# Performance work log

Measured on AMD Instinct MI355X. Metric: run time of the kernel, lower is better.

The kernel has to match this reference:

```python
import jax, jax.numpy as jnp
import numpy as np

N = 10000      # nodes
E = 160000     # directed edges (self loops added inside reference)
IN = 512       # input_len
HID = 256      # hidden per-head dim (hard-coded in module)
OUT = 128      # dim
H = 4          # heads
NEG_SLOPE = 0.2


def setup_inputs() -> dict:
    key = jax.random.key(0)
    ks = jax.random.split(key, 10)
    s = 0.05
    return {
        "x": jax.random.normal(ks[0], (N, IN), dtype=jnp.float32),
        "edge_index": jax.random.randint(ks[1], (2, E), 0, N, dtype=jnp.int64),
        # layer 1 params: GATv2Conv(IN, HID, heads=H, concat=False)
        "Wl1": jax.random.normal(ks[2], (IN, H * HID), dtype=jnp.float32) * s,
        "Wr1": jax.random.normal(ks[3], (IN, H * HID), dtype=jnp.float32) * s,
        "att1": jax.random.normal(ks[4], (H, HID), dtype=jnp.float32) * s,
        "b1": jnp.zeros((HID,), dtype=jnp.float32),
        # layer 2 params: GATv2Conv(HID, OUT, heads=H, concat=False)
        "Wl2": jax.random.normal(ks[5], (HID, H * OUT), dtype=jnp.float32) * s,
        "Wr2": jax.random.normal(ks[6], (HID, H * OUT), dtype=jnp.float32) * s,
        "att2": jax.random.normal(ks[7], (H, OUT), dtype=jnp.float32) * s,
        "b2": jnp.zeros((OUT,), dtype=jnp.float32),
    }


def gatv2_layer(x, src, dst, Wl, Wr, att, bias, num_nodes):
    """PyG GATv2Conv with concat=False (mean over heads), negative_slope=0.2."""
    heads, c = att.shape
    xl = (x @ Wl).reshape(num_nodes, heads, c)   # source transform
    xr = (x @ Wr).reshape(num_nodes, heads, c)   # target transform
    # per-edge attention logits: a^T LeakyReLU(xl[src] + xr[dst])  -> [E, H]
    e = jax.nn.leaky_relu(xl[src] + xr[dst], negative_slope=NEG_SLOPE)
    logits = jnp.einsum('ehc,hc->eh', e, att)
    # segment softmax over incoming edges of each destination node
    m = jax.ops.segment_max(logits, dst, num_segments=num_nodes)   # [N, H]
    ea = jnp.exp(logits - m[dst])
    denom = jax.ops.segment_sum(ea, dst, num_segments=num_nodes)   # [N, H]
    alpha = ea / denom[dst]                                        # [E, H]
    # scatter-aggregate messages
    out = jax.ops.segment_sum(alpha[:, :, None] * xl[src], dst, num_segments=num_nodes)
    return out.mean(axis=1) + bias                                 # [N, C]


def reference(x, edge_index, Wl1, Wr1, att1, b1, Wl2, Wr2, att2, b2):
    num_nodes = x.shape[0]
    loop = jnp.arange(num_nodes, dtype=edge_index.dtype)
    src = jnp.concatenate([edge_index[0], loop])
    dst = jnp.concatenate([edge_index[1], loop])
    h1 = jax.nn.leaky_relu(gatv2_layer(x, src, dst, Wl1, Wr1, att1, b1, num_nodes),
                           negative_slope=NEG_SLOPE)
    h2 = jnp.tanh(gatv2_layer(h1, src, dst, Wl2, Wr2, att2, b2, num_nodes))
    return h2
```

## Files before the change

kernel.cpp:

```cpp
#include <hip/hip_runtime.h>
#include <hip/hip_bf16.h>
#include <math.h>

#define DEVINL __device__ __forceinline__

typedef __attribute__((ext_vector_type(8))) short bf16x8;
typedef __attribute__((ext_vector_type(8))) unsigned short u16x8;
typedef __attribute__((ext_vector_type(4))) float f32x4;

DEVINL float lrelu(float x) { return x > 0.f ? x : 0.2f * x; }

DEVINL unsigned short f2bf_rne(float f) {
    unsigned u = __float_as_uint(f);
    unsigned r = u + 0x7fff + ((u >> 16) & 1);
    return (unsigned short)(r >> 16);
}
DEVINL float bf2f(unsigned short h) { return __uint_as_float(((unsigned)h) << 16); }

DEVINL void gload_lds16(const void* g, void* l) {
    __builtin_amdgcn_global_load_lds(
        (const __attribute__((address_space(1))) void*)g,
        (__attribute__((address_space(3))) void*)l, 16, 0, 0);
}


__global__ void build_edges(const int* __restrict__ ei, int E, int N,
                            int* __restrict__ src, int* __restrict__ dst,
                            int* __restrict__ counts) {
    int e = blockIdx.x * 256 + threadIdx.x;
    int ET = E + N;
    if (e >= ET) return;
    int s, d;
    if (e < E) { s = ei[e]; d = ei[E + e]; }
    else       { s = d = e - E; }
    s = min(max(s, 0), N - 1);
    d = min(max(d, 0), N - 1);
    src[e] = s;
    dst[e] = d;
    atomicAdd(&counts[d], 1);
}

__global__ void scan_offsets(const int* __restrict__ counts, int* __restrict__ offsets, int N) {
    const int T = 1024;
    __shared__ int sums[T];
    int t = threadIdx.x;
    int chunk = (N + T - 1) / T;
    int base = t * chunk;
    int local[16];
    int s = 0;
    for (int i = 0; i < chunk; ++i) {
        int v = (base + i < N) ? counts[base + i] : 0;
        local[i] = s;
        s += v;
    }
    sums[t] = s;
    __syncthreads();
    for (int d = 1; d < T; d <<= 1) {
        int v = (t >= d) ? sums[t - d] : 0;
        __syncthreads();
        sums[t] += v;
        __syncthreads();
    }
    int excl = (t == 0) ? 0 : sums[t - 1];
    for (int i = 0; i < chunk; ++i)
        if (base + i < N) offsets[base + i] = excl + local[i];
    if (t == T - 1) offsets[N] = excl + s;
}

__global__ void fill_eids(const int* __restrict__ src, const int* __restrict__ dst,
                          const int* __restrict__ offsets,
                          int* __restrict__ cursor, int* __restrict__ esrc, int ET) {
    int e = blockIdx.x * 256 + threadIdx.x;
    if (e >= ET) return;
    int d = dst[e];
    int pos = offsets[d] + atomicAdd(&cursor[d], 1);
    esrc[pos] = src[e];
}

__global__ void conv_hi(const float* __restrict__ x, unsigned short* __restrict__ hi,
                        int M, int log2K, int total4) {
    int i = blockIdx.x * 256 + threadIdx.x;
    if (i >= total4) return;
    int e = i * 4;
    int row = e >> log2K;
    ushort4 vh = make_ushort4(0, 0, 0, 0);
    if (row < M) {
        float4 v = *(const float4*)&x[e];
        vh = make_ushort4(f2bf_rne(v.x), f2bf_rne(v.y), f2bf_rne(v.z), f2bf_rne(v.w));
    }
    *(ushort4*)&hi[e] = vh;
}

__global__ void thi(const float* __restrict__ W, unsigned short* __restrict__ BTh,
                    int K, int Nout) {
    __shared__ float tile[32][33];
    int n0 = blockIdx.x * 32, k0 = blockIdx.y * 32;
    int tx = threadIdx.x, ty = threadIdx.y;
#pragma unroll
    for (int i = 0; i < 4; ++i)
        tile[ty + 8 * i][tx] = W[(size_t)(k0 + ty + 8 * i) * Nout + n0 + tx];
    __syncthreads();
#pragma unroll
    for (int i = 0; i < 4; ++i) {
        int r = ty + 8 * i;
        BTh[(size_t)(n0 + r) * K + k0 + tx] = f2bf_rne(tile[tx][r]);
    }
}

template <int TERMS, bool OUTBF16>
__global__ __launch_bounds__(256) void gemm_mfma(
    const unsigned short* __restrict__ Ah, const unsigned short* __restrict__ Al,
    const unsigned short* __restrict__ Bh,
    float* __restrict__ Cf, unsigned short* __restrict__ Cb,
    int M, int Nout, int K) {
    constexpr int BOFF = (TERMS == 2) ? 32768 : 16384;
    __shared__ __align__(16) char lds[BOFF + 16384];
    const int t = threadIdx.x;
    const int L = t & 63, w = t >> 6;
    const int wm = w & 1, wn = w >> 1;
    const int nwg = gridDim.x * gridDim.y;
    int orig = blockIdx.y * gridDim.x + blockIdx.x;
    int q = nwg >> 3, rr = nwg & 7;
    int xcd = orig & 7, pos = orig >> 3;
    int wg = (xcd < rr ? xcd * (q + 1) : rr * (q + 1) + (xcd - rr) * q) + pos;
    const int bm = (wg / gridDim.x) * 128, bn = (wg % gridDim.x) * 128;
    const size_t strideA = (size_t)K * 2;

    const f32x4 vzero = {0.f, 0.f, 0.f, 0.f};
    f32x4 acc[4][4];
#pragma unroll
    for (int i = 0; i < 4; ++i)
#pragma unroll
        for (int j = 0; j < 4; ++j) acc[i][j] = vzero;

    for (int k0 = 0; k0 < K; k0 += 64) {
#pragma unroll
        for (int i = 0; i < 4; ++i) {
            int slot = i * 256 + t;
            int offs = slot * 16;
            int r = offs >> 7;
            int cb = (offs & 127) ^ ((r & 7) << 4);
            size_t gofs = (size_t)r * strideA + (size_t)k0 * 2 + cb;
            gload_lds16((const char*)Ah + (size_t)bm * strideA + gofs, lds + offs);
            if constexpr (TERMS == 2)
                gload_lds16((const char*)Al + (size_t)bm * strideA + gofs, lds + 16384 + offs);
            gload_lds16((const char*)Bh + (size_t)bn * strideA + gofs, lds + BOFF + offs);
        }
        __syncthreads();
#pragma unroll
        for (int kf = 0; kf < 2; ++kf) {
            const int kb = kf * 64 + ((L >> 4) * 16);
            bf16x8 ah[4], al[4], bh[4];
#pragma unroll
            for (int mi = 0; mi < 4; ++mi) {
                int r = wm * 64 + mi * 16 + (L & 15);
                int off = r * 128 + (kb ^ ((r & 7) << 4));
                ah[mi] = *(const bf16x8*)(lds + off);
                if constexpr (TERMS == 2) al[mi] = *(const bf16x8*)(lds + 16384 + off);
            }
#pragma unroll
            for (int ni = 0; ni < 4; ++ni) {
                int r = wn * 64 + ni * 16 + (L & 15);
                int off = r * 128 + (kb ^ ((r & 7) << 4));
                bh[ni] = *(const bf16x8*)(lds + BOFF + off);
            }
#pragma unroll
            for (int mi = 0; mi < 4; ++mi)
#pragma unroll
                for (int ni = 0; ni < 4; ++ni) {
                    acc[mi][ni] = __builtin_amdgcn_mfma_f32_16x16x32_bf16(ah[mi], bh[ni], acc[mi][ni], 0, 0, 0);
                    if constexpr (TERMS == 2)
                        acc[mi][ni] = __builtin_amdgcn_mfma_f32_16x16x32_bf16(al[mi], bh[ni], acc[mi][ni], 0, 0, 0);
                }
        }
        __syncthreads();
    }
    const int colBase = bn + wn * 64 + (L & 15);
#pragma unroll
    for (int mi = 0; mi < 4; ++mi) {
        int row0 = bm + wm * 64 + mi * 16 + (L >> 4) * 4;
#pragma unroll
        for (int j = 0; j < 4; ++j) {
            int row = row0 + j;
            if (row < M) {
#pragma unroll
                for (int ni = 0; ni < 4; ++ni) {
                    if constexpr (OUTBF16)
                        Cb[(size_t)row * Nout + colBase + ni * 16] = f2bf_rne(acc[mi][ni][j]);
                    else
                        Cf[(size_t)row * Nout + colBase + ni * 16] = acc[mi][ni][j];
                }
            }
        }
    }
}

__global__ __launch_bounds__(128) void agg1(const unsigned short* __restrict__ xlr,
                                            const float* __restrict__ att,
                                            const int* __restrict__ offsets,
                                            const int* __restrict__ esrc,
                                            const float* __restrict__ bias,
                                            unsigned short* __restrict__ outH,
                                            unsigned short* __restrict__ outL,
                                            int N) {
    __shared__ float accLds[4][256];
    const int t = threadIdx.x;
    const int wv = t >> 6, lane = t & 63;
    const int n = blockIdx.x;

    if (n >= N) {
        int c = t * 2;
        *(ushort2*)&outH[(size_t)n * 256 + c] = make_ushort2(0, 0);
        *(ushort2*)&outL[(size_t)n * 256 + c] = make_ushort2(0, 0);
        return;
    }

    const int eoff = 512 * wv + lane * 8;
    const int h = eoff >> 8;
    const int gl = lane & 31;

    float a[8];
    {
        const float* pa = att + h * 256 + gl * 8;
        float4 a0 = *(const float4*)pa, a1 = *(const float4*)(pa + 4);
        a[0] = a0.x; a[1] = a0.y; a[2] = a0.z; a[3] = a0.w;
        a[4] = a1.x; a[5] = a1.y; a[6] = a1.z; a[7] = a1.w;
    }
    float r[8];
    {
        u16x8 u = *(const u16x8*)(xlr + (size_t)n * 2048 + 1024 + eoff);
#pragma unroll
        for (int v = 0; v < 8; ++v) r[v] = bf2f(u[v]);
    }
    int o0 = offsets[n];
    int deg = offsets[n + 1] - o0;

    float acc[8];
#pragma unroll
    for (int v = 0; v < 8; ++v) acc[v] = 0.f;
    float s = 0.f;

    for (int j = 0; j < deg; j += 2) {
        int e0 = esrc[o0 + j];
        bool has1 = (j + 1) < deg;
        int e1 = esrc[o0 + (has1 ? j + 1 : j)];
        u16x8 g0 = *(const u16x8*)(xlr + (size_t)e0 * 2048 + eoff);
        u16x8 g1 = *(const u16x8*)(xlr + (size_t)e1 * 2048 + eoff);
        float x0[8], x1[8];
#pragma unroll
        for (int v = 0; v < 8; ++v) { x0[v] = bf2f(g0[v]); x1[v] = bf2f(g1[v]); }
        float q0 = 0.f, q1 = 0.f;
#pragma unroll
        for (int v = 0; v < 8; ++v) {
            q0 += a[v] * lrelu(x0[v] + r[v]);
            q1 += a[v] * lrelu(x1[v] + r[v]);
        }
#pragma unroll
        for (int m = 1; m < 32; m <<= 1) {
            q0 += __shfl_xor(q0, m);
            q1 += __shfl_xor(q1, m);
        }
        q0 = fminf(fmaxf(q0, -60.f), 60.f);
        q1 = fminf(fmaxf(q1, -60.f), 60.f);
        float w0 = __expf(q0);
        float w1 = has1 ? __expf(q1) : 0.f;
        s += w0 + w1;
#pragma unroll
        for (int v = 0; v < 8; ++v) acc[v] += w0 * x0[v] + w1 * x1[v];
    }

    float inv = 1.0f / s;
#pragma unroll
    for (int v = 0; v < 8; ++v) accLds[h][gl * 8 + v] = acc[v] * inv;
    __syncthreads();

    {
        int c0 = t, c1 = t + 128;
        float v0 = (accLds[0][c0] + accLds[1][c0] + accLds[2][c0] + accLds[3][c0]) * 0.25f + bias[c0];
        float v1 = (accLds[0][c1] + accLds[1][c1] + accLds[2][c1] + accLds[3][c1]) * 0.25f + bias[c1];
        v0 = lrelu(v0); v1 = lrelu(v1);
        unsigned short h0 = f2bf_rne(v0), h1v = f2bf_rne(v1);
        outH[(size_t)n * 256 + c0] = h0;
        outH[(size_t)n * 256 + c1] = h1v;
        outL[(size_t)n * 256 + c0] = f2bf_rne(v0 - bf2f(h0));
        outL[(size_t)n * 256 + c1] = f2bf_rne(v1 - bf2f(h1v));
    }
}

__global__ __launch_bounds__(256) void agg2(const unsigned short* __restrict__ xlr,
                                            const float* __restrict__ att,
                                            const int* __restrict__ offsets,
                                            const int* __restrict__ esrc,
                                            const float* __restrict__ bias,
                                            float* __restrict__ out, int N) {
    const int lane = threadIdx.x & 63;
    const int n = blockIdx.x * 4 + (threadIdx.x >> 6);
    if (n >= N) return;
    const int h = lane >> 4, gl = lane & 15;
    const int eoff = lane * 8;

    float a[8], bs[8];
    {
        const float* pa = att + h * 128 + gl * 8;
        float4 a0 = *(const float4*)pa, a1 = *(const float4*)(pa + 4);
        a[0] = a0.x; a[1] = a0.y; a[2] = a0.z; a[3] = a0.w;
        a[4] = a1.x; a[5] = a1.y; a[6] = a1.z; a[7] = a1.w;
        const float* pb = bias + gl * 8;
        float4 b0 = *(const float4*)pb, b1v = *(const float4*)(pb + 4);
        bs[0] = b0.x; bs[1] = b0.y; bs[2] = b0.z; bs[3] = b0.w;
        bs[4] = b1v.x; bs[5] = b1v.y; bs[6] = b1v.z; bs[7] = b1v.w;
    }
    float r[8];
    {
        u16x8 u = *(const u16x8*)(xlr + (size_t)n * 1024 + 512 + eoff);
#pragma unroll
        for (int v = 0; v < 8; ++v) r[v] = bf2f(u[v]);
    }
    int o0 = offsets[n];
    int deg = offsets[n + 1] - o0;

    float acc[8];
#pragma unroll
    for (int v = 0; v < 8; ++v) acc[v] = 0.f;
    float s = 0.f;

    for (int j = 0; j < deg; j += 2) {
        int e0 = esrc[o0 + j];
        bool has1 = (j + 1) < deg;
        int e1 = esrc[o0 + (has1 ? j + 1 : j)];
        u16x8 g0 = *(const u16x8*)(xlr + (size_t)e0 * 1024 + eoff);
        u16x8 g1 = *(const u16x8*)(xlr + (size_t)e1 * 1024 + eoff);
        float x0[8], x1[8];
#pragma unroll
        for (int v = 0; v < 8; ++v) { x0[v] = bf2f(g0[v]); x1[v] = bf2f(g1[v]); }
        float q0 = 0.f, q1 = 0.f;
#pragma unroll
        for (int v = 0; v < 8; ++v) {
            q0 += a[v] * lrelu(x0[v] + r[v]);
            q1 += a[v] * lrelu(x1[v] + r[v]);
        }
#pragma unroll
        for (int m = 1; m < 16; m <<= 1) {
            q0 += __shfl_xor(q0, m);
            q1 += __shfl_xor(q1, m);
        }
        q0 = fminf(fmaxf(q0, -60.f), 60.f);
        q1 = fminf(fmaxf(q1, -60.f), 60.f);
        float w0 = __expf(q0);
        float w1 = has1 ? __expf(q1) : 0.f;
        s += w0 + w1;
#pragma unroll
        for (int v = 0; v < 8; ++v) acc[v] += w0 * x0[v] + w1 * x1[v];
    }

    float inv = 1.0f / s;
#pragma unroll
    for (int v = 0; v < 8; ++v) acc[v] *= inv;
#pragma unroll
    for (int v = 0; v < 8; ++v) {
        acc[v] += __shfl_xor(acc[v], 16);
        acc[v] += __shfl_xor(acc[v], 32);
    }
    if (h == 0) {
        float o[8];
#pragma unroll
        for (int v = 0; v < 8; ++v) o[v] = tanhf(acc[v] * 0.25f + bs[v]);
        float* po = out + (size_t)n * 128 + gl * 8;
        *(float4*)po = make_float4(o[0], o[1], o[2], o[3]);
        *(float4*)(po + 4) = make_float4(o[4], o[5], o[6], o[7]);
    }
}


extern "C" void kernel_launch(void* const* d_in, const int* in_sizes, int n_in,
                              void* d_out, int out_size, void* d_ws, size_t ws_size,
                              hipStream_t stream) {
    const float* x    = (const float*)d_in[0];
    const int*   ei   = (const int*)d_in[1];
    const float* Wl1  = (const float*)d_in[2];
    const float* Wr1  = (const float*)d_in[3];
    const float* att1 = (const float*)d_in[4];
    const float* b1   = (const float*)d_in[5];
    const float* Wl2  = (const float*)d_in[6];
    const float* Wr2  = (const float*)d_in[7];
    const float* att2 = (const float*)d_in[8];
    const float* b2   = (const float*)d_in[9];
    float* out = (float*)d_out;

    const int IN = 512, HID = 256, OUT = 128, H = 4;
    int N  = in_sizes[0] / IN;
    int E  = in_sizes[1] / 2;
    int ET = E + N;
    int M2 = ((N + 127) / 128) * 128;

    char* w = (char*)d_ws;
    auto carve = [&](size_t bytes) {
        char* p = w;
        w += (bytes + 255) & ~(size_t)255;
        return (void*)p;
    };
    unsigned short* x_hi = (unsigned short*)carve((size_t)M2 * IN * 2);
    unsigned short* xlr1 = (unsigned short*)carve((size_t)N * 2 * H * HID * 2);
    unsigned short* BT1 = (unsigned short*)carve((size_t)(2 * H * HID) * IN * 2);
    int* src     = (int*)carve((size_t)ET * 4);
    int* dst     = (int*)carve((size_t)ET * 4);
    int* counts  = (int*)carve((size_t)N * 4);
    int* cursor  = (int*)carve((size_t)N * 4);
    int* offsets = (int*)carve((size_t)(N + 1) * 4);
    int* esrc    = (int*)carve((size_t)ET * 4);
    unsigned short* h1_h = x_hi;
    unsigned short* h1_l = x_hi + (size_t)M2 * HID;
    unsigned short* xlr2 = xlr1;
    unsigned short* BT2  = BT1;

    hipMemsetAsync(counts, 0, (size_t)((char*)offsets - (char*)counts), stream);
    build_edges<<<(ET + 255) / 256, 256, 0, stream>>>(ei, E, N, src, dst, counts);
    scan_offsets<<<1, 1024, 0, stream>>>(counts, offsets, N);
    fill_eids<<<(ET + 255) / 256, 256, 0, stream>>>(src, dst, offsets, cursor, esrc, ET);

    {
        int total4 = M2 * IN / 4;
        conv_hi<<<(total4 + 255) / 256, 256, 0, stream>>>(x, x_hi, N, 9, total4);
        thi<<<dim3((H * HID) / 32, IN / 32), dim3(32, 8), 0, stream>>>(Wl1, BT1, IN, H * HID);
        thi<<<dim3((H * HID) / 32, IN / 32), dim3(32, 8), 0, stream>>>(Wr1, BT1 + (size_t)(H * HID) * IN, IN, H * HID);
    }
    {
        dim3 g((2 * H * HID) / 128, M2 / 128);
        gemm_mfma<1, true><<<g, 256, 0, stream>>>(x_hi, nullptr, BT1, nullptr, xlr1, N, 2 * H * HID, IN);
    }
    agg1<<<M2, 128, 0, stream>>>(xlr1, att1, offsets, esrc, b1, h1_h, h1_l, N);
    thi<<<dim3((H * OUT) / 32, HID / 32), dim3(32, 8), 0, stream>>>(Wl2, BT2, HID, H * OUT);
    thi<<<dim3((H * OUT) / 32, HID / 32), dim3(32, 8), 0, stream>>>(Wr2, BT2 + (size_t)(H * OUT) * HID, HID, H * OUT);
    {
        dim3 g((2 * H * OUT) / 128, M2 / 128);
        gemm_mfma<2, true><<<g, 256, 0, stream>>>(h1_h, h1_l, BT2, nullptr, xlr2, N, 2 * H * OUT, HID);
    }
    agg2<<<(N + 3) / 4, 256, 0, stream>>>(xlr2, att2, offsets, esrc, b2, out, N);
}
```

Before: 186.3 us.

## Pack two nodes per agg1 block, use DPP reductions and packed float math

Several micro-optimisations land together. Pairs of transpose launches are merged into one thi2 launch using blockIdx.z. agg1 now handles two nodes per 256-thread block, with vectorised ushort2 stores. In both aggregation kernels, neighbor indices are made wave-uniform with readfirstlane, shuffle reductions become DPP row sums, and bf16 unpacking plus arithmetic uses packed float2 operations. The aim is to cut launch count, per-block overhead and ALU/shuffle cost in the gather loops, at the price of more complex code and reliance on uniform degrees within each wave.

```diff
diff --git a/kernel.cpp b/kernel.cpp
--- a/kernel.cpp
+++ b/kernel.cpp
@@ -7,6 +7,7 @@
 typedef __attribute__((ext_vector_type(8))) short bf16x8;
 typedef __attribute__((ext_vector_type(8))) unsigned short u16x8;
 typedef __attribute__((ext_vector_type(4))) float f32x4;
+typedef __attribute__((ext_vector_type(2))) float f32x2;
 
 DEVINL float lrelu(float x) { return x > 0.f ? x : 0.2f * x; }
 
@@ -16,6 +17,26 @@
     return (unsigned short)(r >> 16);
 }
 DEVINL float bf2f(unsigned short h) { return __uint_as_float(((unsigned)h) << 16); }
+
+DEVINL f32x2 bf2f2(unsigned u) {
+    f32x2 r;
+    r.x = __uint_as_float(u << 16);
+    r.y = __uint_as_float(u & 0xffff0000u);
+    return r;
+}
+
+template <int CTRL>
+DEVINL float dppadd(float x) {
+    return x + __int_as_float(__builtin_amdgcn_update_dpp(
+        0, __float_as_int(x), CTRL, 0xF, 0xF, false));
+}
+DEVINL float rowsum16(float x) {
+    x = dppadd<0x121>(x);
+    x = dppadd<0x122>(x);
+    x = dppadd<0x124>(x);
+    x = dppadd<0x128>(x);
+    return x;
+}
 
 DEVINL void gload_lds16(const void* g, void* l) {
     __builtin_amdgcn_global_load_lds(
@@ -91,9 +112,11 @@
     *(ushort4*)&hi[e] = vh;
 }
 
-__global__ void thi(const float* __restrict__ W, unsigned short* __restrict__ BTh,
-                    int K, int Nout) {
+__global__ void thi2(const float* __restrict__ W0, const float* __restrict__ W1,
+                     unsigned short* __restrict__ BT, int K, int Nout) {
     __shared__ float tile[32][33];
+    const float* W = blockIdx.z ? W1 : W0;
+    unsigned short* out = BT + (size_t)blockIdx.z * Nout * K;
     int n0 = blockIdx.x * 32, k0 = blockIdx.y * 32;
     int tx = threadIdx.x, ty = threadIdx.y;
 #pragma unroll
@@ -103,7 +126,7 @@
 #pragma unroll
     for (int i = 0; i < 4; ++i) {
         int r = ty + 8 * i;
-        BTh[(size_t)(n0 + r) * K + k0 + tx] = f2bf_rne(tile[tx][r]);
+        out[(size_t)(n0 + r) * K + k0 + tx] = f2bf_rne(tile[tx][r]);
     }
 }
 
@@ -195,7 +218,7 @@
     }
 }
 
-__global__ __launch_bounds__(128) void agg1(const unsigned short* __restrict__ xlr,
+__global__ __launch_bounds__(256) void agg1(const unsigned short* __restrict__ xlr,
                                             const float* __restrict__ att,
                                             const int* __restrict__ offsets,
                                             const int* __restrict__ esrc,
@@ -203,13 +226,15 @@
                                             unsigned short* __restrict__ outH,
                                             unsigned short* __restrict__ outL,
                                             int N) {
-    __shared__ float accLds[4][256];
+    __shared__ float accLds[2][4][256];
     const int t = threadIdx.x;
-    const int wv = t >> 6, lane = t & 63;
-    const int n = blockIdx.x;
-
-    if (n >= N) {
-        int c = t * 2;
+    const int half = t >> 7;
+    const int ht = t & 127;
+    const int wv = ht >> 6, lane = ht & 63;
+    const int n = blockIdx.x * 2 + half;
+
+    if (blockIdx.x * 2 >= N) {
+        int c = ht * 2;
         *(ushort2*)&outH[(size_t)n * 256 + c] = make_ushort2(0, 0);
         *(ushort2*)&outL[(size_t)n * 256 + c] = make_ushort2(0, 0);
         return;
@@ -219,71 +244,80 @@
     const int h = eoff >> 8;
     const int gl = lane & 31;
 
-    float a[8];
+    f32x2 a2[4], r2[4];
     {
         const float* pa = att + h * 256 + gl * 8;
-        float4 a0 = *(const float4*)pa, a1 = *(const float4*)(pa + 4);
-        a[0] = a0.x; a[1] = a0.y; a[2] = a0.z; a[3] = a0.w;
-        a[4] = a1.x; a[5] = a1.y; a[6] = a1.z; a[7] = a1.w;
-    }
-    float r[8];
-    {
-        u16x8 u = *(const u16x8*)(xlr + (size_t)n * 2048 + 1024 + eoff);
-#pragma unroll
-        for (int v = 0; v < 8; ++v) r[v] = bf2f(u[v]);
-    }
-    int o0 = offsets[n];
-    int deg = offsets[n + 1] - o0;
-
-    float acc[8];
-#pragma unroll
-    for (int v = 0; v < 8; ++v) acc[v] = 0.f;
+#pragma unroll
+        for (int p = 0; p < 4; ++p) { a2[p].x = pa[2 * p]; a2[p].y = pa[2 * p + 1]; }
+        const uint4 u = *(const uint4*)(xlr + (size_t)n * 2048 + 1024 + eoff);
+        r2[0] = bf2f2(u.x); r2[1] = bf2f2(u.y); r2[2] = bf2f2(u.z); r2[3] = bf2f2(u.w);
+    }
+    const int o0  = __builtin_amdgcn_readfirstlane(offsets[n]);
+    const int deg = __builtin_amdgcn_readfirstlane(offsets[n + 1]) - o0;
+
+    f32x2 acc2[4];
+#pragma unroll
+    for (int p = 0; p < 4; ++p) acc2[p] = (f32x2){0.f, 0.f};
     float s = 0.f;
 
     for (int j = 0; j < deg; j += 2) {
-        int e0 = esrc[o0 + j];
+        int e0 = __builtin_amdgcn_readfirstlane(esrc[o0 + j]);
         bool has1 = (j + 1) < deg;
-        int e1 = esrc[o0 + (has1 ? j + 1 : j)];
-        u16x8 g0 = *(const u16x8*)(xlr + (size_t)e0 * 2048 + eoff);
-        u16x8 g1 = *(const u16x8*)(xlr + (size_t)e1 * 2048 + eoff);
-        float x0[8], x1[8];
-#pragma unroll
-        for (int v = 0; v < 8; ++v) { x0[v] = bf2f(g0[v]); x1[v] = bf2f(g1[v]); }
-        float q0 = 0.f, q1 = 0.f;
-#pragma unroll
-        for (int v = 0; v < 8; ++v) {
-            q0 += a[v] * lrelu(x0[v] + r[v]);
-            q1 += a[v] * lrelu(x1[v] + r[v]);
-        }
-#pragma unroll
-        for (int m = 1; m < 32; m <<= 1) {
-            q0 += __shfl_xor(q0, m);
-            q1 += __shfl_xor(q1, m);
-        }
+        int e1 = __builtin_amdgcn_readfirstlane(esrc[o0 + (has1 ? j + 1 : j)]);
+        const unsigned short* row0 = xlr + (size_t)e0 * 2048;
+        const unsigned short* row1 = xlr + (size_t)e1 * 2048;
+        uint4 g0 = *(const uint4*)(row0 + eoff);
+        uint4 g1 = *(const uint4*)(row1 + eoff);
+        f32x2 x0[4], x1[4];
+        x0[0] = bf2f2(g0.x); x0[1] = bf2f2(g0.y); x0[2] = bf2f2(g0.z); x0[3] = bf2f2(g0.w);
+        x1[0] = bf2f2(g1.x); x1[1] = bf2f2(g1.y); x1[2] = bf2f2(g1.z); x1[3] = bf2f2(g1.w);
+        f32x2 q02 = {0.f, 0.f}, q12 = {0.f, 0.f};
+#pragma unroll
+        for (int p = 0; p < 4; ++p) {
+            f32x2 t0 = x0[p] + r2[p];
+            f32x2 t1 = x1[p] + r2[p];
+            f32x2 m0 = t0 * 0.2f;
+            f32x2 m1 = t1 * 0.2f;
+            f32x2 u0, u1;
+            u0.x = fmaxf(t0.x, m0.x); u0.y = fmaxf(t0.y, m0.y);
+            u1.x = fmaxf(t1.x, m1.x); u1.y = fmaxf(t1.y, m1.y);
+            q02 += a2[p] * u0;
+            q12 += a2[p] * u1;
+        }
+        float q0 = q02.x + q02.y;
+        float q1 = q12.x + q12.y;
+        q0 = rowsum16(q0); q0 += __shfl_xor(q0, 16);
+        q1 = rowsum16(q1); q1 += __shfl_xor(q1, 16);
         q0 = fminf(fmaxf(q0, -60.f), 60.f);
         q1 = fminf(fmaxf(q1, -60.f), 60.f);
         float w0 = __expf(q0);
         float w1 = has1 ? __expf(q1) : 0.f;
         s += w0 + w1;
-#pragma unroll
-        for (int v = 0; v < 8; ++v) acc[v] += w0 * x0[v] + w1 * x1[v];
+        f32x2 w02 = {w0, w0}, w12 = {w1, w1};
+#pragma unroll
+        for (int p = 0; p < 4; ++p) acc2[p] += x0[p] * w02 + x1[p] * w12;
     }
 
     float inv = 1.0f / s;
-#pragma unroll
-    for (int v = 0; v < 8; ++v) accLds[h][gl * 8 + v] = acc[v] * inv;
+    {
+        float* dst = &accLds[half][h][gl * 8];
+#pragma unroll
+        for (int p = 0; p < 4; ++p) {
+            dst[2 * p]     = acc2[p].x * inv;
+            dst[2 * p + 1] = acc2[p].y * inv;
+        }
+    }
     __syncthreads();
 
     {
-        int c0 = t, c1 = t + 128;
-        float v0 = (accLds[0][c0] + accLds[1][c0] + accLds[2][c0] + accLds[3][c0]) * 0.25f + bias[c0];
-        float v1 = (accLds[0][c1] + accLds[1][c1] + accLds[2][c1] + accLds[3][c1]) * 0.25f + bias[c1];
+        int c = ht * 2;
+        float v0 = (accLds[half][0][c] + accLds[half][1][c] + accLds[half][2][c] + accLds[half][3][c]) * 0.25f + bias[c];
+        float v1 = (accLds[half][0][c + 1] + accLds[half][1][c + 1] + accLds[half][2][c + 1] + accLds[half][3][c + 1]) * 0.25f + bias[c + 1];
         v0 = lrelu(v0); v1 = lrelu(v1);
         unsigned short h0 = f2bf_rne(v0), h1v = f2bf_rne(v1);
-        outH[(size_t)n * 256 + c0] = h0;
-        outH[(size_t)n * 256 + c1] = h1v;
-        outL[(size_t)n * 256 + c0] = f2bf_rne(v0 - bf2f(h0));
-        outL[(size_t)n * 256 + c1] = f2bf_rne(v1 - bf2f(h1v));
+        *(ushort2*)&outH[(size_t)n * 256 + c] = make_ushort2(h0, h1v);
+        *(ushort2*)&outL[(size_t)n * 256 + c] =
+            make_ushort2(f2bf_rne(v0 - bf2f(h0)), f2bf_rne(v1 - bf2f(h1v)));
     }
 }
 
@@ -299,72 +333,78 @@
     const int h = lane >> 4, gl = lane & 15;
     const int eoff = lane * 8;
 
-    float a[8], bs[8];
+    f32x2 a2[4], bs2[4], r2[4];
     {
         const float* pa = att + h * 128 + gl * 8;
-        float4 a0 = *(const float4*)pa, a1 = *(const float4*)(pa + 4);
-        a[0] = a0.x; a[1] = a0.y; a[2] = a0.z; a[3] = a0.w;
-        a[4] = a1.x; a[5] = a1.y; a[6] = a1.z; a[7] = a1.w;
         const float* pb = bias + gl * 8;
-        float4 b0 = *(const float4*)pb, b1v = *(const float4*)(pb + 4);
-        bs[0] = b0.x; bs[1] = b0.y; bs[2] = b0.z; bs[3] = b0.w;
-        bs[4] = b1v.x; bs[5] = b1v.y; bs[6] = b1v.z; bs[7] = b1v.w;
-    }
-    float r[8];
-    {
-        u16x8 u = *(const u16x8*)(xlr + (size_t)n * 1024 + 512 + eoff);
-#pragma unroll
-        for (int v = 0; v < 8; ++v) r[v] = bf2f(u[v]);
-    }
-    int o0 = offsets[n];
-    int deg = offsets[n + 1] - o0;
-
-    float acc[8];
-#pragma unroll
-    for (int v = 0; v < 8; ++v) acc[v] = 0.f;
+#pragma unroll
+        for (int p = 0; p < 4; ++p) {
+            a2[p].x = pa[2 * p];  a2[p].y = pa[2 * p + 1];
+            bs2[p].x = pb[2 * p]; bs2[p].y = pb[2 * p + 1];
+        }
+        const uint4 u = *(const uint4*)(xlr + (size_t)n * 1024 + 512 + eoff);
+        r2[0] = bf2f2(u.x); r2[1] = bf2f2(u.y); r2[2] = bf2f2(u.z); r2[3] = bf2f2(u.w);
+    }
+    const int o0  = __builtin_amdgcn_readfirstlane(offsets[n]);
+    const int deg = __builtin_amdgcn_readfirstlane(offsets[n + 1]) - o0;
+
+    f32x2 acc2[4];
+#pragma unroll
+    for (int p = 0; p < 4; ++p) acc2[p] = (f32x2){0.f, 0.f};
     float s = 0.f;
 
     for (int j = 0; j < deg; j += 2) {
-        int e0 = esrc[o0 + j];
+        int e0 = __builtin_amdgcn_readfirstlane(esrc[o0 + j]);
         bool has1 = (j + 1) < deg;
-        int e1 = esrc[o0 + (has1 ? j + 1 : j)];
-        u16x8 g0 = *(const u16x8*)(xlr + (size_t)e0 * 1024 + eoff);
-        u16x8 g1 = *(const u16x8*)(xlr + (size_t)e1 * 1024 + eoff);
-        float x0[8], x1[8];
-#pragma unroll
-        for (int v = 0; v < 8; ++v) { x0[v] = bf2f(g0[v]); x1[v] = bf2f(g1[v]); }
-        float q0 = 0.f, q1 = 0.f;
-#pragma unroll
-        for (int v = 0; v < 8; ++v) {
-            q0 += a[v] * lrelu(x0[v] + r[v]);
-            q1 += a[v] * lrelu(x1[v] + r[v]);
-        }
-#pragma unroll
-        for (int m = 1; m < 16; m <<= 1) {
-            q0 += __shfl_xor(q0, m);
-            q1 += __shfl_xor(q1, m);
-        }
+        int e1 = __builtin_amdgcn_readfirstlane(esrc[o0 + (has1 ? j + 1 : j)]);
+        const unsigned short* row0 = xlr + (size_t)e0 * 1024;
+        const unsigned short* row1 = xlr + (size_t)e1 * 1024;
+        uint4 g0 = *(const uint4*)(row0 + eoff);
+        uint4 g1 = *(const uint4*)(row1 + eoff);
+        f32x2 x0[4], x1[4];
+        x0[0] = bf2f2(g0.x); x0[1] = bf2f2(g0.y); x0[2] = bf2f2(g0.z); x0[3] = bf2f2(g0.w);
+        x1[0] = bf2f2(g1.x); x1[1] = bf2f2(g1.y); x1[2] = bf2f2(g1.z); x1[3] = bf2f2(g1.w);
+        f32x2 q02 = {0.f, 0.f}, q12 = {0.f, 0.f};
+#pragma unroll
+        for (int p = 0; p < 4; ++p) {
+            f32x2 t0 = x0[p] + r2[p];
+            f32x2 t1 = x1[p] + r2[p];
+            f32x2 m0 = t0 * 0.2f;
+            f32x2 m1 = t1 * 0.2f;
+            f32x2 u0, u1;
+            u0.x = fmaxf(t0.x, m0.x); u0.y = fmaxf(t0.y, m0.y);
+            u1.x = fmaxf(t1.x, m1.x); u1.y = fmaxf(t1.y, m1.y);
+            q02 += a2[p] * u0;
+            q12 += a2[p] * u1;
+        }
+        float q0 = rowsum16(q02.x + q02.y);
+        float q1 = rowsum16(q12.x + q12.y);
         q0 = fminf(fmaxf(q0, -60.f), 60.f);
         q1 = fminf(fmaxf(q1, -60.f), 60.f);
         float w0 = __expf(q0);
         float w1 = has1 ? __expf(q1) : 0.f;
         s += w0 + w1;
-#pragma unroll
-        for (int v = 0; v < 8; ++v) acc[v] += w0 * x0[v] + w1 * x1[v];
+        f32x2 w02 = {w0, w0}, w12 = {w1, w1};
+#pragma unroll
+        for (int p = 0; p < 4; ++p) acc2[p] += x0[p] * w02 + x1[p] * w12;
     }
 
     float inv = 1.0f / s;
 #pragma unroll
-    for (int v = 0; v < 8; ++v) acc[v] *= inv;
-#pragma unroll
-    for (int v = 0; v < 8; ++v) {
-        acc[v] += __shfl_xor(acc[v], 16);
-        acc[v] += __shfl_xor(acc[v], 32);
+    for (int p = 0; p < 4; ++p) {
+        acc2[p].x *= inv; acc2[p].y *= inv;
+        acc2[p].x += __shfl_xor(acc2[p].x, 16);
+        acc2[p].x += __shfl_xor(acc2[p].x, 32);
+        acc2[p].y += __shfl_xor(acc2[p].y, 16);
+        acc2[p].y += __shfl_xor(acc2[p].y, 32);
     }
     if (h == 0) {
         float o[8];
 #pragma unroll
-        for (int v = 0; v < 8; ++v) o[v] = tanhf(acc[v] * 0.25f + bs[v]);
+        for (int p = 0; p < 4; ++p) {
+            o[2 * p]     = tanhf(acc2[p].x * 0.25f + bs2[p].x);
+            o[2 * p + 1] = tanhf(acc2[p].y * 0.25f + bs2[p].y);
+        }
         float* po = out + (size_t)n * 128 + gl * 8;
         *(float4*)po = make_float4(o[0], o[1], o[2], o[3]);
         *(float4*)(po + 4) = make_float4(o[4], o[5], o[6], o[7]);
@@ -421,16 +461,14 @@
     {
         int total4 = M2 * IN / 4;
         conv_hi<<<(total4 + 255) / 256, 256, 0, stream>>>(x, x_hi, N, 9, total4);
-        thi<<<dim3((H * HID) / 32, IN / 32), dim3(32, 8), 0, stream>>>(Wl1, BT1, IN, H * HID);
-        thi<<<dim3((H * HID) / 32, IN / 32), dim3(32, 8), 0, stream>>>(Wr1, BT1 + (size_t)(H * HID) * IN, IN, H * HID);
+        thi2<<<dim3((H * HID) / 32, IN / 32, 2), dim3(32, 8), 0, stream>>>(Wl1, Wr1, BT1, IN, H * HID);
     }
     {
         dim3 g((2 * H * HID) / 128, M2 / 128);
         gemm_mfma<1, true><<<g, 256, 0, stream>>>(x_hi, nullptr, BT1, nullptr, xlr1, N, 2 * H * HID, IN);
     }
-    agg1<<<M2, 128, 0, stream>>>(xlr1, att1, offsets, esrc, b1, h1_h, h1_l, N);
-    thi<<<dim3((H * OUT) / 32, HID / 32), dim3(32, 8), 0, stream>>>(Wl2, BT2, HID, H * OUT);
-    thi<<<dim3((H * OUT) / 32, HID / 32), dim3(32, 8), 0, stream>>>(Wr2, BT2 + (size_t)(H * OUT) * HID, HID, H * OUT);
+    agg1<<<M2 / 2, 256, 0, stream>>>(xlr1, att1, offsets, esrc, b1, h1_h, h1_l, N);
+    thi2<<<dim3((H * OUT) / 32, HID / 32, 2), dim3(32, 8), 0, stream>>>(Wl2, Wr2, BT2, HID, H * OUT);
     {
         dim3 g((2 * H * OUT) / 128, M2 / 128);
         gemm_mfma<2, true><<<g, 256, 0, stream>>>(h1_h, h1_l, BT2, nullptr, xlr2, N, 2 * H * OUT, HID);
```

Measured after the change: 171.2 us. 1.09x faster.
